# Kernel tuning notes

Hardware: AMD Instinct MI355X
Metric: run time of the kernel (lower is better)

## Reference

```python
import jax, jax.numpy as jnp
import numpy as np

N_NODES = 50000; N_EDGES = 800000
N_GRAPHS = 50; NODES_PER_GRAPH = 1000  # equal-size graphs: to_dense_batch == reshape
D_UNI = 1024; PE = 16; CH = 80; E_EMB = 16
D_STATE = 16; D_CONV = 4; DT_RANK = 5  # ceil(80/16)


def sinpe(pos, d):
    # interleaved sin/cos: even cols sin, odd cols cos
    den = jnp.power(10000.0, 2.0 * jnp.arange(d // 2, dtype=jnp.float32) / d)
    ang = pos[:, None] / den
    return jnp.stack([jnp.sin(ang), jnp.cos(ang)], -1).reshape(pos.shape[0], d)


def batchnorm(h, w, b, m, v):
    # eval-mode BatchNorm1d with running stats
    return (h - m) * jax.lax.rsqrt(v + 1e-5) * w + b


def gat_conv(x, src, dst, eattr, W, att_s, att_d, W_e, att_e, bias):
    # PyG GATConv (heads=1, add_self_loops=True, fill_value='mean', eval mode)
    N = x.shape[0]
    cnt = jax.ops.segment_sum(jnp.ones(src.shape[0], x.dtype), dst, N)
    loop_attr = jax.ops.segment_sum(eattr, dst, N) / jnp.maximum(cnt, 1.0)[:, None]
    idx = jnp.arange(N, dtype=src.dtype)
    src = jnp.concatenate([src, idx]); dst = jnp.concatenate([dst, idx])
    ea = jnp.concatenate([eattr, loop_attr], 0)
    h = x @ W                                   # [N, CH]
    a_s = h @ att_s; a_d = h @ att_d            # [N]
    a_e = (ea @ W_e) @ att_e                    # [E+N]
    alpha = jax.nn.leaky_relu(a_s[src] + a_d[dst] + a_e, negative_slope=0.2)
    amax = jax.ops.segment_max(alpha, dst, N)   # every node has a self loop
    ex = jnp.exp(alpha - amax[dst])
    denom = jax.ops.segment_sum(ex, dst, N)
    w = ex / denom[dst]
    out = jax.ops.segment_sum(w[:, None] * h[src], dst, N)
    return out + bias


def mamba(h, in_W, conv_w, conv_b, xp_W, dt_W, dt_b, A_log, D_p, out_W):
    # mamba_ssm Mamba(d_model=CH, d_state=16, d_conv=4, expand=1), all linears bias-free
    B, L, _ = h.shape
    xz = h @ in_W                               # [B, L, 2*CH]
    xc, z = jnp.split(xz, 2, -1)
    xpad = jnp.pad(xc, ((0, 0), (D_CONV - 1, 0), (0, 0)))
    xconv = conv_b
    for k in range(D_CONV):                     # depthwise causal conv, K=4
        xconv = xconv + xpad[:, k:k + L, :] * conv_w[:, k]
    u = jax.nn.silu(xconv)                      # [B, L, CH]
    proj = u @ xp_W                             # [B, L, DT_RANK + 2*D_STATE]
    dt, Bm, Cm = jnp.split(proj, [DT_RANK, DT_RANK + D_STATE], -1)
    dt = jax.nn.softplus(dt @ dt_W + dt_b)      # [B, L, CH]
    A = -jnp.exp(A_log)                         # [CH, D_STATE]
    dA = jnp.exp(dt[..., None] * A)             # [B, L, CH, D_STATE]
    dBu = dt[..., None] * Bm[:, :, None, :] * u[..., None]

    def step(hst, inp):
        dA_t, dBu_t, C_t = inp
        hst = dA_t * hst + dBu_t                # [B, CH, D_STATE]
        return hst, jnp.einsum('bds,bs->bd', hst, C_t)

    h0 = jnp.zeros((B, xc.shape[-1], D_STATE), h.dtype)
    _, ys = jax.lax.scan(step, h0, (jnp.moveaxis(dA, 1, 0), jnp.moveaxis(dBu, 1, 0), jnp.moveaxis(Cm, 1, 0)))
    y = jnp.moveaxis(ys, 0, 1) + u * D_p
    y = y * jax.nn.silu(z)
    return y @ out_W


def _forward(x, edge_index, ea_cat, ea_cont, W_uni, b_uni, edge_emb, W_edge, b_edge,
             gat_W, gat_as, gat_ad, gat_We, gat_ae, gat_b,
             bn1_w, bn1_b, bn1_m, bn1_v, bn2_w, bn2_b, bn2_m, bn2_v, bn3_w, bn3_b, bn3_m, bn3_v,
             m_in_W, m_conv_w, m_conv_b, m_xp_W, m_dt_W, m_dt_b, m_Alog, m_D, m_out_W,
             mlp_W1, mlp_b1, mlp_W2, mlp_b2, f_W1, f_b1, f_W2, f_b2, f_W3, f_b3):
    xf = x[:, 2:2 + D_UNI] @ W_uni + b_uni      # [N, 64]
    pe = jnp.concatenate([sinpe(x[:, 0], PE // 2), sinpe(x[:, 1], PE // 2)], -1)
    h = jnp.concatenate([xf, pe], 1)            # [N, 80]
    eattr = ea_cont @ W_edge + b_edge + edge_emb[ea_cat]
    src, dst = edge_index[0], edge_index[1]
    # GATMambaBlock (eval: dropouts identity)
    hg = gat_conv(h, src, dst, eattr, gat_W, gat_as, gat_ad, gat_We, gat_ae, gat_b)
    hg = batchnorm(hg, bn1_w, bn1_b, bn1_m, bn1_v)
    hd = h.reshape(N_GRAPHS, NODES_PER_GRAPH, CH)
    hm = mamba(hd, m_in_W, m_conv_w, m_conv_b, m_xp_W, m_dt_W, m_dt_b, m_Alog, m_D, m_out_W)
    hm = batchnorm(hm.reshape(N_NODES, CH), bn2_w, bn2_b, bn2_m, bn2_v)
    out = hg + hm
    out = out + (jax.nn.relu(out @ mlp_W1 + mlp_b1) @ mlp_W2 + mlp_b2)
    out = batchnorm(out, bn3_w, bn3_b, bn3_m, bn3_v)
    out = jax.nn.relu(out)
    pooled = out.reshape(N_GRAPHS, NODES_PER_GRAPH, CH).mean(1)  # global_mean_pool
    h1 = jax.nn.relu(pooled @ f_W1 + f_b1)
    h2 = jax.nn.relu(h1 @ f_W2 + f_b2)
    pred = h2 @ f_W3 + f_b3
    return pred, pooled


def setup_inputs() -> dict:
    ks = iter(jax.random.split(jax.random.key(0), 64))
    def nrm(shape, scale):
        return jax.random.normal(next(ks), shape, jnp.float32) * scale
    inp = {}
    inp['x'] = jnp.concatenate([jax.random.uniform(next(ks), (N_NODES, 2)) * 100.0,
                                nrm((N_NODES, D_UNI), 1.0)], 1)
    inp['edge_index'] = jax.random.randint(next(ks), (2, N_EDGES), 0, N_NODES, jnp.int32)
    inp['ea_cat'] = jax.random.randint(next(ks), (N_EDGES,), 0, 21, jnp.int32)
    inp['ea_cont'] = nrm((N_EDGES, 2), 1.0)
    inp['W_uni'] = nrm((D_UNI, 64), 0.03); inp['b_uni'] = jnp.zeros((64,))
    inp['edge_emb'] = nrm((21, E_EMB), 1.0)
    inp['W_edge'] = nrm((2, E_EMB), 0.5); inp['b_edge'] = jnp.zeros((E_EMB,))
    inp['gat_W'] = nrm((CH, CH), 0.1); inp['gat_as'] = nrm((CH,), 0.1); inp['gat_ad'] = nrm((CH,), 0.1)
    inp['gat_We'] = nrm((E_EMB, CH), 0.1); inp['gat_ae'] = nrm((CH,), 0.1); inp['gat_b'] = jnp.zeros((CH,))
    for i in (1, 2, 3):
        inp[f'bn{i}_w'] = jnp.ones((CH,)); inp[f'bn{i}_b'] = jnp.zeros((CH,))
        inp[f'bn{i}_m'] = nrm((CH,), 0.1)
        inp[f'bn{i}_v'] = jax.random.uniform(next(ks), (CH,), minval=0.5, maxval=1.5)
    inp['m_in_W'] = nrm((CH, 2 * CH), 0.1)
    inp['m_conv_w'] = nrm((CH, D_CONV), 0.3); inp['m_conv_b'] = jnp.zeros((CH,))
    inp['m_xp_W'] = nrm((CH, DT_RANK + 2 * D_STATE), 0.1)
    inp['m_dt_W'] = nrm((DT_RANK, CH), 0.3); inp['m_dt_b'] = nrm((CH,), 0.1)
    inp['m_Alog'] = jnp.log(jnp.tile(jnp.arange(1, D_STATE + 1, dtype=jnp.float32), (CH, 1)))
    inp['m_D'] = jnp.ones((CH,)); inp['m_out_W'] = nrm((CH, CH), 0.1)
    inp['mlp_W1'] = nrm((CH, 2 * CH), 0.1); inp['mlp_b1'] = jnp.zeros((2 * CH,))
    inp['mlp_W2'] = nrm((2 * CH, CH), 0.1); inp['mlp_b2'] = jnp.zeros((CH,))
    inp['f_W1'] = nrm((CH, CH // 2), 0.15); inp['f_b1'] = jnp.zeros((CH // 2,))
    inp['f_W2'] = nrm((CH // 2, CH // 4), 0.2); inp['f_b2'] = jnp.zeros((CH // 4,))
    inp['f_W3'] = nrm((CH // 4, 1), 0.3); inp['f_b3'] = jnp.zeros((1,))
    return inp


def reference(x, edge_index, ea_cat, ea_cont, W_uni, b_uni, edge_emb, W_edge, b_edge,
              gat_W, gat_as, gat_ad, gat_We, gat_ae, gat_b,
              bn1_w, bn1_b, bn1_m, bn1_v, bn2_w, bn2_b, bn2_m, bn2_v, bn3_w, bn3_b, bn3_m, bn3_v,
              m_in_W, m_conv_w, m_conv_b, m_xp_W, m_dt_W, m_dt_b, m_Alog, m_D, m_out_W,
              mlp_W1, mlp_b1, mlp_W2, mlp_b2, f_W1, f_b1, f_W2, f_b2, f_W3, f_b3):
    return _forward(x, edge_index, ea_cat, ea_cont, W_uni, b_uni, edge_emb, W_edge, b_edge,
                    gat_W, gat_as, gat_ad, gat_We, gat_ae, gat_b,
                    bn1_w, bn1_b, bn1_m, bn1_v, bn2_w, bn2_b, bn2_m, bn2_v, bn3_w, bn3_b, bn3_m, bn3_v,
                    m_in_W, m_conv_w, m_conv_b, m_xp_W, m_dt_W, m_dt_b, m_Alog, m_D, m_out_W,
                    mlp_W1, mlp_b1, mlp_W2, mlp_b2, f_W1, f_b1, f_W2, f_b2, f_W3, f_b3)
```

## Files before the change

### kernel.cpp

```cpp
#include <hip/hip_runtime.h>
#include <hip/hip_bf16.h>
#include <cstdint>

#define NNODES 50000
#define NEDGES 800000
#define NGRAPHS 50
#define NPG 1000
#define NB_SCAN 196
#define NCHUNK 10
#define CLEN 100

#define CO_WEAE 0
#define CO_WEC2 16
#define CO_BES  18
#define CO_EMBS 20
#define CO_WS   48
#define CO_WD   128
#define CO_BN1S 208
#define CO_BN1SH 288
#define CO_BN2S 368
#define CO_BN2SH 448
#define CO_BN3S 528
#define CO_BN3SH 608

__device__ __forceinline__ float lrelu(float x){ return x >= 0.f ? x : 0.2f*x; }
__device__ __forceinline__ float siluf(float x){ return x / (1.f + __expf(-x)); }

__device__ __forceinline__ int wave_incl_scan(int v) {
    int lane = threadIdx.x & 63;
    #pragma unroll
    for (int d = 1; d < 64; d <<= 1) {
        int o = __shfl_up(v, d, 64);
        if (lane >= d) v += o;
    }
    return v;
}

__global__ __launch_bounds__(256) void k_precompute(
        const float* __restrict__ gat_W, const float* __restrict__ gat_as, const float* __restrict__ gat_ad,
        const float* __restrict__ gat_We, const float* __restrict__ gat_ae,
        const float* __restrict__ W_edge, const float* __restrict__ b_edge, const float* __restrict__ edge_emb,
        const float* __restrict__ bn1_w, const float* __restrict__ bn1_b, const float* __restrict__ bn1_m, const float* __restrict__ bn1_v,
        const float* __restrict__ bn2_w, const float* __restrict__ bn2_b, const float* __restrict__ bn2_m, const float* __restrict__ bn2_v,
        const float* __restrict__ bn3_w, const float* __restrict__ bn3_b, const float* __restrict__ bn3_m, const float* __restrict__ bn3_v,
        float* __restrict__ consts)
{
    __shared__ float weae[16];
    int tid = threadIdx.x;
    if (tid < 16) {
        float s = 0.f;
        for (int c = 0; c < 80; ++c) s += gat_We[tid*80 + c] * gat_ae[c];
        weae[tid] = s;
        consts[CO_WEAE + tid] = s;
    }
    __syncthreads();
    if (tid < 2) {
        float s = 0.f;
        for (int k = 0; k < 16; ++k) s += W_edge[tid*16 + k] * weae[k];
        consts[CO_WEC2 + tid] = s;
    } else if (tid == 2) {
        float s = 0.f;
        for (int k = 0; k < 16; ++k) s += b_edge[k] * weae[k];
        consts[CO_BES] = s;
    }
    if (tid >= 32 && tid < 53) {
        int j = tid - 32;
        float s = 0.f;
        for (int k = 0; k < 16; ++k) s += edge_emb[j*16 + k] * weae[k];
        consts[CO_EMBS + j] = s;
    }
    if (tid >= 64 && tid < 144) {
        int r = tid - 64;
        float s1 = 0.f, s2 = 0.f;
        for (int c = 0; c < 80; ++c) {
            float w = gat_W[r*80 + c];
            s1 += w * gat_as[c];
            s2 += w * gat_ad[c];
        }
        consts[CO_WS + r] = s1;
        consts[CO_WD + r] = s2;
    }
    if (tid >= 160 && tid < 240) {
        int c = tid - 160;
        float sc1 = bn1_w[c] / sqrtf(bn1_v[c] + 1e-5f);
        consts[CO_BN1S + c] = sc1; consts[CO_BN1SH + c] = bn1_b[c] - bn1_m[c]*sc1;
        float sc2 = bn2_w[c] / sqrtf(bn2_v[c] + 1e-5f);
        consts[CO_BN2S + c] = sc2; consts[CO_BN2SH + c] = bn2_b[c] - bn2_m[c]*sc2;
        float sc3 = bn3_w[c] / sqrtf(bn3_v[c] + 1e-5f);
        consts[CO_BN3S + c] = sc3; consts[CO_BN3SH + c] = bn3_b[c] - bn3_m[c]*sc3;
    }
}

__global__ __launch_bounds__(256) void k_feat(const float* __restrict__ x,
        const float* __restrict__ W, const float* __restrict__ b,
        float* __restrict__ h)
{
    __shared__ float As[32][68];
    __shared__ float Bs[32][64];
    int tid = threadIdx.x;
    int node0 = blockIdx.x * 64;
    int tx = tid & 15, ty = tid >> 4;
    float acc[4][4] = {};
    int lr = tid >> 2;
    int lk = (tid & 3) * 8;
    int bk = tid >> 3;
    int bc = (tid & 7) * 8;
    for (int kk = 0; kk < 1024; kk += 32) {
        int n = node0 + lr;
        if (n < NNODES) {
            const float* xp = x + (size_t)n*1026 + 2 + kk + lk;
            #pragma unroll
            for (int j = 0; j < 8; ++j) As[lk+j][lr] = xp[j];
        } else {
            #pragma unroll
            for (int j = 0; j < 8; ++j) As[lk+j][lr] = 0.f;
        }
        const float* wp = W + (size_t)(kk+bk)*64 + bc;
        #pragma unroll
        for (int j = 0; j < 8; ++j) Bs[bk][bc+j] = wp[j];
        __syncthreads();
        #pragma unroll 8
        for (int i = 0; i < 32; ++i) {
            const float4 a  = *(const float4*)&As[i][ty*4];
            const float4 bb = *(const float4*)&Bs[i][tx*4];
            float av[4] = {a.x, a.y, a.z, a.w};
            float bv[4] = {bb.x, bb.y, bb.z, bb.w};
            #pragma unroll
            for (int r = 0; r < 4; ++r)
                #pragma unroll
                for (int j = 0; j < 4; ++j)
                    acc[r][j] = fmaf(av[r], bv[j], acc[r][j]);
        }
        __syncthreads();
    }
    #pragma unroll
    for (int r = 0; r < 4; ++r) {
        int n = node0 + ty*4 + r;
        if (n < NNODES) {
            #pragma unroll
            for (int j = 0; j < 4; ++j) {
                int c = tx*4 + j;
                h[(size_t)n*80 + c] = acc[r][j] + b[c];
            }
        }
    }
    for (int idx = tid; idx < 64*16; idx += 256) {
        int row = idx >> 4, col = idx & 15;
        int n = node0 + row;
        if (n < NNODES) {
            float pos = x[(size_t)n*1026 + (col < 8 ? 0 : 1)];
            int jj = (col & 7) >> 1;
            const float dens[4] = {1.f, 10.f, 100.f, 1000.f};
            float ang = pos / dens[jj];
            float v = (col & 1) ? cosf(ang) : sinf(ang);
            h[(size_t)n*80 + 64 + col] = v;
        }
    }
}

template<int K, int C, int RPT, int EPI>
__global__ __launch_bounds__(320) void k_gemm_rows(const float* __restrict__ in,
        const float* __restrict__ W, float* __restrict__ out, float* __restrict__ out2,
        const float* __restrict__ extra, const float* __restrict__ consts, int N)
{
    constexpr int GROUPS = 320 / C;
    constexpr int NPB = GROUPS * RPT;
    __shared__ float rows[NPB][K];
    int tid = threadIdx.x;
    int n0 = blockIdx.x * NPB;
    for (int idx = tid; idx < NPB*K; idx += 320) {
        int r = idx / K, k = idx - r*K;
        int n = n0 + r;
        rows[r][k] = (n < N) ? in[(size_t)n*K + k] : 0.f;
    }
    __syncthreads();
    int c = tid % C, grp = tid / C;
    float acc[RPT];
    #pragma unroll
    for (int r = 0; r < RPT; ++r) acc[r] = 0.f;
    #pragma unroll 4
    for (int k = 0; k < K; ++k) {
        float w = W[(size_t)k*C + c];
        #pragma unroll
        for (int r = 0; r < RPT; ++r) acc[r] = fmaf(rows[grp*RPT + r][k], w, acc[r]);
    }
    #pragma unroll
    for (int r = 0; r < RPT; ++r) {
        int n = n0 + grp*RPT + r;
        if (n >= N) continue;
        float v = acc[r];
        if (EPI == 0) {
            out[(size_t)n*C + c] = v;
        } else if (EPI == 1) {
            if (c < 80) out[(size_t)n*80 + c] = v;
            else        out2[(size_t)n*80 + (c-80)] = siluf(v);
        } else if (EPI == 2) {
            float bv = consts[CO_BN2S + c]*v + consts[CO_BN2SH + c] + extra[(size_t)n*80 + c];
            out[(size_t)n*80 + c] = bv;
        }
    }
}

__global__ __launch_bounds__(256) void k_edge_scalar(const float* __restrict__ ea_cont,
        const int* __restrict__ ea_cat, const int* __restrict__ dst,
        const float* __restrict__ consts, float* __restrict__ a_e,
        float* __restrict__ sum_ae, int* __restrict__ cnt)
{
    int e = blockIdx.x * 256 + threadIdx.x;
    if (e >= NEDGES) return;
    float2 ec = ((const float2*)ea_cont)[e];
    float v = ec.x*consts[CO_WEC2] + ec.y*consts[CO_WEC2+1] + consts[CO_BES]
            + consts[CO_EMBS + ea_cat[e]];
    a_e[e] = v;
    int d = dst[e];
    atomicAdd(sum_ae + d, v);
    atomicAdd(cnt + d, 1);
}

__global__ __launch_bounds__(256) void k_node_as(const float* __restrict__ h,
        const float* __restrict__ consts, const float* __restrict__ sum_ae,
        const int* __restrict__ cnt, float* __restrict__ a_s, float* __restrict__ a_d,
        float* __restrict__ alpha_self)
{
    __shared__ float wsv[80], wdv[80];
    int tid = threadIdx.x;
    if (tid < 80) { wsv[tid] = consts[CO_WS + tid]; wdv[tid] = consts[CO_WD + tid]; }
    __syncthreads();
    int n = blockIdx.x * 256 + tid;
    if (n >= NNODES) return;
    const float4* hr = (const float4*)(h + (size_t)n*80);
    float as = 0.f, ad = 0.f;
    #pragma unroll 5
    for (int i = 0; i < 20; ++i) {
        float4 f = hr[i];
        as += f.x*wsv[i*4] + f.y*wsv[i*4+1] + f.z*wsv[i*4+2] + f.w*wsv[i*4+3];
        ad += f.x*wdv[i*4] + f.y*wdv[i*4+1] + f.z*wdv[i*4+2] + f.w*wdv[i*4+3];
    }
    float aes = sum_ae[n] / fmaxf((float)cnt[n], 1.f);
    a_s[n] = as; a_d[n] = ad;
    alpha_self[n] = lrelu(as + ad + aes);
}

__global__ __launch_bounds__(256) void k_psum1(const int* __restrict__ cnt, int* __restrict__ bsum)
{
    __shared__ int ws4[4];
    int tid = threadIdx.x;
    int n = blockIdx.x*256 + tid;
    int v = (n < NNODES) ? cnt[n] : 0;
    int s = wave_incl_scan(v);
    if ((tid & 63) == 63) ws4[tid >> 6] = s;
    __syncthreads();
    if (tid == 0) {
        int t = 0;
        for (int w = 0; w < 4; ++w) t += ws4[w];
        bsum[blockIdx.x] = t;
    }
}

__global__ __launch_bounds__(256) void k_psum2(int* __restrict__ bsum)
{
    __shared__ int wsum[4], woff[4];
    int tid = threadIdx.x;
    int v = (tid < NB_SCAN) ? bsum[tid] : 0;
    int s = wave_incl_scan(v);
    if ((tid & 63) == 63) wsum[tid >> 6] = s;
    __syncthreads();
    if (tid == 0) { int r = 0; for (int w = 0; w < 4; ++w) { woff[w] = r; r += wsum[w]; } }
    __syncthreads();
    int excl = s - v + woff[tid >> 6];
    if (tid < NB_SCAN) bsum[tid] = excl;
}

__global__ __launch_bounds__(256) void k_psum3(const int* __restrict__ cnt,
        const int* __restrict__ bsum, int* __restrict__ rowptr, int* __restrict__ cursor)
{
    __shared__ int wsum[4], woff[4];
    int tid = threadIdx.x;
    int n = blockIdx.x*256 + tid;
    int v = (n < NNODES) ? cnt[n] : 0;
    int s = wave_incl_scan(v);
    if ((tid & 63) == 63) wsum[tid >> 6] = s;
    __syncthreads();
    if (tid == 0) { int r = 0; for (int w = 0; w < 4; ++w) { woff[w] = r; r += wsum[w]; } }
    __syncthreads();
    int excl = s - v + woff[tid >> 6] + bsum[blockIdx.x];
    if (n < NNODES) { rowptr[n] = excl; cursor[n] = excl; }
}

__global__ __launch_bounds__(256) void k_bucket(const int* __restrict__ src,
        const int* __restrict__ dst, const float* __restrict__ a_s,
        const float* __restrict__ a_d, const float* __restrict__ a_e,
        int* __restrict__ cursor, int2* __restrict__ ebuf)
{
    int e = blockIdx.x*256 + threadIdx.x;
    if (e >= NEDGES) return;
    int sN = src[e], d = dst[e];
    float al = lrelu(a_s[sN] + a_d[d] + a_e[e]);
    int pos = atomicAdd(cursor + d, 1);
    ebuf[pos] = make_int2(sN, __float_as_int(al));
}

__global__ __launch_bounds__(256) void k_gat_agg(const int* __restrict__ rowptr,
        const int* __restrict__ cnt, const int2* __restrict__ ebuf,
        const float* __restrict__ alpha_self, const float* __restrict__ hg,
        const float* __restrict__ gat_b, const float* __restrict__ consts,
        float* __restrict__ hgbn)
{
    int tid = threadIdx.x;
    int grp = tid >> 4, l = tid & 15;
    int n = blockIdx.x*16 + grp;
    if (n >= NNODES) return;
    int r0 = rowptr[n], c = cnt[n];
    float aself = alpha_self[n];
    float m = aself;
    for (int i = l; i < c; i += 16)
        m = fmaxf(m, __int_as_float(ebuf[r0 + i].y));
    m = fmaxf(m, __shfl_xor(m, 1, 16));
    m = fmaxf(m, __shfl_xor(m, 2, 16));
    m = fmaxf(m, __shfl_xor(m, 4, 16));
    m = fmaxf(m, __shfl_xor(m, 8, 16));
    float ex0 = __expf(aself - m);
    float denom = ex0;
    float acc[5];
    const float* hn = hg + (size_t)n*80;
    #pragma unroll
    for (int j = 0; j < 5; ++j) acc[j] = ex0 * hn[l + 16*j];
    for (int i = 0; i < c; ++i) {
        int2 p = ebuf[r0 + i];
        float ex = __expf(__int_as_float(p.y) - m);
        denom += ex;
        const float* hs = hg + (size_t)p.x*80;
        #pragma unroll
        for (int j = 0; j < 5; ++j) acc[j] = fmaf(ex, hs[l + 16*j], acc[j]);
    }
    float inv = 1.f/denom;
    #pragma unroll
    for (int j = 0; j < 5; ++j) {
        int ch = l + 16*j;
        float v = acc[j]*inv + gat_b[ch];
        hgbn[(size_t)n*80 + ch] = consts[CO_BN1S + ch]*v + consts[CO_BN1SH + ch];
    }
}

__global__ __launch_bounds__(256) void k_conv_proj(const float* __restrict__ xc,
        const float* __restrict__ conv_w, const float* __restrict__ conv_b,
        const float* __restrict__ xp_W, const float* __restrict__ dt_W,
        const float* __restrict__ dt_b, float* __restrict__ u_g,
        float* __restrict__ Bm, float* __restrict__ Cm, float* __restrict__ dt_g)
{
    __shared__ float us[40][80];
    __shared__ float dtr[40][5];
    int g = blockIdx.x / 25, chunk = blockIdx.x % 25;
    int t0 = chunk * 40;
    int tid = threadIdx.x;
    size_t gbase = (size_t)g * NPG;
    for (int idx = tid; idx < 40*80; idx += 256) {
        int t = idx / 80, d = idx - t*80;
        int tt = t0 + t;
        float acc = conv_b[d];
        #pragma unroll
        for (int k = 0; k < 4; ++k) {
            int ti = tt - 3 + k;
            float xv = (ti >= 0) ? xc[(gbase + ti)*80 + d] : 0.f;
            acc = fmaf(xv, conv_w[d*4 + k], acc);
        }
        float uv = siluf(acc);
        us[t][d] = uv;
        u_g[(gbase + tt)*80 + d] = uv;
    }
    __syncthreads();
    for (int idx = tid; idx < 40*37; idx += 256) {
        int t = idx / 37, j = idx - t*37;
        float acc = 0.f;
        #pragma unroll 4
        for (int k = 0; k < 80; ++k) acc = fmaf(us[t][k], xp_W[k*37 + j], acc);
        int tt = t0 + t;
        if (j < 5) dtr[t][j] = acc;
        else if (j < 21) Bm[(gbase + tt)*16 + (j-5)] = acc;
        else Cm[(gbase + tt)*16 + (j-21)] = acc;
    }
    __syncthreads();
    for (int idx = tid; idx < 40*80; idx += 256) {
        int t = idx / 80, d = idx - t*80;
        float acc = dt_b[d];
        #pragma unroll
        for (int r = 0; r < 5; ++r) acc = fmaf(dtr[t][r], dt_W[r*80 + d], acc);
        float sp = (acc > 20.f) ? acc : log1pf(__expf(acc));
        dt_g[(gbase + t0 + t)*80 + d] = sp;
    }
}

__global__ __launch_bounds__(256) void k_scan_a(const float* __restrict__ dt,
        const float* __restrict__ u, const float* __restrict__ Bm,
        const float* __restrict__ A_log, float* __restrict__ Pb, float* __restrict__ Qb)
{
    int b = blockIdx.x;
    int c = b % NCHUNK; int gd = b / NCHUNK;
    int g = gd / 5, dblk = gd % 5;
    int dl = threadIdx.x >> 4, s = threadIdx.x & 15;
    int d = dblk*16 + dl;
    float a = -__expf(A_log[d*16 + s]);
    size_t base80 = (size_t)g*NPG*80 + (size_t)c*CLEN*80 + d;
    size_t base16 = (size_t)g*NPG*16 + (size_t)c*CLEN*16 + s;
    float P = 1.f, Q = 0.f;
    for (int t = 0; t < CLEN; ++t) {
        float dtv = dt[base80 + (size_t)t*80];
        float uv  = u [base80 + (size_t)t*80];
        float Bv  = Bm[base16 + (size_t)t*16];
        float dA = __expf(dtv * a);
        Q = fmaf(dA, Q, dtv*uv*Bv);
        P *= dA;
    }
    size_t o = ((size_t)(g*NCHUNK + c)*80 + d)*16 + s;
    Pb[o] = P; Qb[o] = Q;
}

__global__ __launch_bounds__(256) void k_scan_c(const float* __restrict__ dt,
        const float* __restrict__ u, const float* __restrict__ Bm,
        const float* __restrict__ Cm, const float* __restrict__ A_log,
        const float* __restrict__ Dp, const float* __restrict__ sz,
        const float* __restrict__ Pb, const float* __restrict__ Qb,
        float* __restrict__ yraw)
{
    int b = blockIdx.x;
    int c = b % NCHUNK; int gd = b / NCHUNK;
    int g = gd / 5, dblk = gd % 5;
    int dl = threadIdx.x >> 4, s = threadIdx.x & 15;
    int d = dblk*16 + dl;
    float a = -__expf(A_log[d*16 + s]);
    float Dd = Dp[d];
    float hst = 0.f;
    for (int cc = 0; cc < c; ++cc) {
        size_t o = ((size_t)(g*NCHUNK + cc)*80 + d)*16 + s;
        hst = fmaf(Pb[o], hst, Qb[o]);
    }
    size_t base80 = (size_t)g*NPG*80 + (size_t)c*CLEN*80 + d;
    size_t base16 = (size_t)g*NPG*16 + (size_t)c*CLEN*16 + s;
    for (int t = 0; t < CLEN; ++t) {
        float dtv = dt[base80 + (size_t)t*80];
        float uv  = u [base80 + (size_t)t*80];
        float Bv  = Bm[base16 + (size_t)t*16];
        float Cv  = Cm[base16 + (size_t)t*16];
        float dA = __expf(dtv * a);
        hst = fmaf(dA, hst, dtv*uv*Bv);
        float cv = hst * Cv;
        cv += __shfl_xor(cv, 1, 16);
        cv += __shfl_xor(cv, 2, 16);
        cv += __shfl_xor(cv, 4, 16);
        cv += __shfl_xor(cv, 8, 16);
        if (s == 0) {
            size_t i = base80 + (size_t)t*80;
            yraw[i] = (cv + uv*Dd) * sz[i];
        }
    }
}

__global__ __launch_bounds__(640) void k_mlp(const float* __restrict__ s1,
        const float* __restrict__ W1, const float* __restrict__ b1,
        const float* __restrict__ W2, const float* __restrict__ b2,
        const float* __restrict__ consts, float* __restrict__ pooled)
{
    __shared__ float s1s[4][80];
    __shared__ float t1s[4][160];
    int tid = threadIdx.x;
    int n0 = blockIdx.x * 4;
    if (tid < 320) {
        int r = tid / 80, c = tid - r*80;
        s1s[r][c] = s1[(size_t)(n0 + r)*80 + c];
    }
    __syncthreads();
    {
        int r = tid / 160, j = tid - (tid/160)*160;
        float acc = b1[j];
        #pragma unroll 4
        for (int k = 0; k < 80; ++k) acc = fmaf(s1s[r][k], W1[k*160 + j], acc);
        t1s[r][j] = fmaxf(acc, 0.f);
    }
    __syncthreads();
    if (tid < 320) {
        int r = tid / 80, c = tid - (tid/80)*80;
        float acc = b2[c];
        #pragma unroll 4
        for (int k = 0; k < 160; ++k) acc = fmaf(t1s[r][k], W2[k*80 + c], acc);
        float v = s1s[r][c] + acc;
        v = consts[CO_BN3S + c]*v + consts[CO_BN3SH + c];
        v = fmaxf(v, 0.f);
        s1s[r][c] = v;
    }
    __syncthreads();
    if (tid < 80) {
        float sum = s1s[0][tid] + s1s[1][tid] + s1s[2][tid] + s1s[3][tid];
        atomicAdd(pooled + (n0 / NPG)*80 + tid, sum);
    }
}

__global__ __launch_bounds__(256) void k_pool_final(const float* __restrict__ pooled,
        const float* __restrict__ f_W1, const float* __restrict__ f_b1,
        const float* __restrict__ f_W2, const float* __restrict__ f_b2,
        const float* __restrict__ f_W3, const float* __restrict__ f_b3,
        float* __restrict__ d_out)
{
    __shared__ float pl[50*80];
    __shared__ float h1[50*40];
    __shared__ float h2[50*20];
    int tid = threadIdx.x;
    for (int idx = tid; idx < 50*80; idx += 256) {
        float v = pooled[idx] * (1.f/NPG);
        pl[idx] = v;
        d_out[50 + idx] = v;
    }
    __syncthreads();
    for (int idx = tid; idx < 50*40; idx += 256) {
        int g = idx / 40, j = idx - g*40;
        float acc = f_b1[j];
        for (int k = 0; k < 80; ++k) acc = fmaf(pl[g*80+k], f_W1[k*40+j], acc);
        h1[idx] = fmaxf(acc, 0.f);
    }
    __syncthreads();
    for (int idx = tid; idx < 50*20; idx += 256) {
        int g = idx / 20, j = idx - g*20;
        float acc = f_b2[j];
        for (int k = 0; k < 40; ++k) acc = fmaf(h1[g*40+k], f_W2[k*20+j], acc);
        h2[idx] = fmaxf(acc, 0.f);
    }
    __syncthreads();
    if (tid < 50) {
        float acc = f_b3[0];
        for (int k = 0; k < 20; ++k) acc = fmaf(h2[tid*20+k], f_W3[k], acc);
        d_out[tid] = acc;
    }
}

extern "C" void kernel_launch(void* const* d_in, const int* in_sizes, int n_in,
                              void* d_out, int out_size, void* d_ws, size_t ws_size,
                              hipStream_t stream)
{
    (void)in_sizes; (void)n_in; (void)out_size; (void)ws_size;
    const float* x        = (const float*)d_in[0];
    const int*   eidx     = (const int*)d_in[1];
    const int*   ea_cat   = (const int*)d_in[2];
    const float* ea_cont  = (const float*)d_in[3];
    const float* W_uni    = (const float*)d_in[4];
    const float* b_uni    = (const float*)d_in[5];
    const float* edge_emb = (const float*)d_in[6];
    const float* W_edge   = (const float*)d_in[7];
    const float* b_edge   = (const float*)d_in[8];
    const float* gat_W    = (const float*)d_in[9];
    const float* gat_as   = (const float*)d_in[10];
    const float* gat_ad   = (const float*)d_in[11];
    const float* gat_We   = (const float*)d_in[12];
    const float* gat_ae   = (const float*)d_in[13];
    const float* gat_b    = (const float*)d_in[14];
    const float* bn1_w = (const float*)d_in[15]; const float* bn1_b = (const float*)d_in[16];
    const float* bn1_m = (const float*)d_in[17]; const float* bn1_v = (const float*)d_in[18];
    const float* bn2_w = (const float*)d_in[19]; const float* bn2_b = (const float*)d_in[20];
    const float* bn2_m = (const float*)d_in[21]; const float* bn2_v = (const float*)d_in[22];
    const float* bn3_w = (const float*)d_in[23]; const float* bn3_b = (const float*)d_in[24];
    const float* bn3_m = (const float*)d_in[25]; const float* bn3_v = (const float*)d_in[26];
    const float* m_in_W   = (const float*)d_in[27];
    const float* m_conv_w = (const float*)d_in[28];
    const float* m_conv_b = (const float*)d_in[29];
    const float* m_xp_W   = (const float*)d_in[30];
    const float* m_dt_W   = (const float*)d_in[31];
    const float* m_dt_b   = (const float*)d_in[32];
    const float* m_Alog   = (const float*)d_in[33];
    const float* m_D      = (const float*)d_in[34];
    const float* m_out_W  = (const float*)d_in[35];
    const float* mlp_W1 = (const float*)d_in[36]; const float* mlp_b1 = (const float*)d_in[37];
    const float* mlp_W2 = (const float*)d_in[38]; const float* mlp_b2 = (const float*)d_in[39];
    const float* f_W1 = (const float*)d_in[40]; const float* f_b1 = (const float*)d_in[41];
    const float* f_W2 = (const float*)d_in[42]; const float* f_b2 = (const float*)d_in[43];
    const float* f_W3 = (const float*)d_in[44]; const float* f_b3 = (const float*)d_in[45];

    const int* src = eidx;
    const int* dst = eidx + NEDGES;

    float* wsf = (float*)d_ws;
    const size_t NN80 = (size_t)NNODES*80;
    size_t O_CONSTS = 0;
    size_t O_SUMAE  = 1024;
    size_t O_CNT    = O_SUMAE + NNODES;
    size_t O_POOLED = O_CNT + NNODES;
    size_t O_AE     = O_POOLED + 4000;
    size_t O_AS     = O_AE + NEDGES;
    size_t O_AD     = O_AS + NNODES;
    size_t O_ASELF  = O_AD + NNODES;
    size_t O_ROWPTR = O_ASELF + NNODES;
    size_t O_CURSOR = O_ROWPTR + NNODES;
    size_t O_BSUM   = O_CURSOR + NNODES;
    size_t O_EBUF   = O_BSUM + 256;
    size_t O_PB     = O_EBUF;
    size_t O_QB     = O_EBUF + 640000;
    size_t O_H      = O_EBUF + 2*(size_t)NEDGES;
    size_t O_HG     = O_H + NN80;
    size_t O_HGBN   = O_HG + NN80;
    size_t O_XC     = O_HGBN + NN80;
    size_t O_SZ     = O_XC + NN80;
    size_t O_U      = O_SZ + NN80;
    size_t O_DT     = O_U + NN80;
    size_t O_BM     = O_DT + NN80;
    size_t O_CM     = O_BM + (size_t)NNODES*16;

    hipMemsetAsync(wsf + O_SUMAE, 0, (2*(size_t)NNODES + 4000)*sizeof(float), stream);

    k_precompute<<<1, 256, 0, stream>>>(gat_W, gat_as, gat_ad, gat_We, gat_ae,
        W_edge, b_edge, edge_emb,
        bn1_w, bn1_b, bn1_m, bn1_v, bn2_w, bn2_b, bn2_m, bn2_v, bn3_w, bn3_b, bn3_m, bn3_v,
        wsf + O_CONSTS);

    k_feat<<<(NNODES + 63)/64, 256, 0, stream>>>(x, W_uni, b_uni, wsf + O_H);

    k_edge_scalar<<<(NEDGES + 255)/256, 256, 0, stream>>>(ea_cont, ea_cat, dst,
        wsf + O_CONSTS, wsf + O_AE, wsf + O_SUMAE, (int*)(wsf + O_CNT));

    k_gemm_rows<80, 80, 8, 0><<<(NNODES + 31)/32, 320, 0, stream>>>(
        wsf + O_H, gat_W, wsf + O_HG, nullptr, nullptr, wsf + O_CONSTS, NNODES);

    k_node_as<<<(NNODES + 255)/256, 256, 0, stream>>>(wsf + O_H, wsf + O_CONSTS,
        wsf + O_SUMAE, (const int*)(wsf + O_CNT), wsf + O_AS, wsf + O_AD, wsf + O_ASELF);

    k_psum1<<<NB_SCAN, 256, 0, stream>>>((const int*)(wsf + O_CNT), (int*)(wsf + O_BSUM));
    k_psum2<<<1, 256, 0, stream>>>((int*)(wsf + O_BSUM));
    k_psum3<<<NB_SCAN, 256, 0, stream>>>((const int*)(wsf + O_CNT),
        (const int*)(wsf + O_BSUM), (int*)(wsf + O_ROWPTR), (int*)(wsf + O_CURSOR));

    k_bucket<<<(NEDGES + 255)/256, 256, 0, stream>>>(src, dst, wsf + O_AS,
        wsf + O_AD, wsf + O_AE, (int*)(wsf + O_CURSOR), (int2*)(wsf + O_EBUF));

    k_gat_agg<<<NNODES/16, 256, 0, stream>>>((const int*)(wsf + O_ROWPTR),
        (const int*)(wsf + O_CNT), (const int2*)(wsf + O_EBUF), wsf + O_ASELF,
        wsf + O_HG, gat_b, wsf + O_CONSTS, wsf + O_HGBN);

    k_gemm_rows<80, 160, 8, 1><<<(NNODES + 15)/16, 320, 0, stream>>>(
        wsf + O_H, m_in_W, wsf + O_XC, wsf + O_SZ, nullptr, wsf + O_CONSTS, NNODES);

    k_conv_proj<<<NGRAPHS*25, 256, 0, stream>>>(wsf + O_XC, m_conv_w, m_conv_b,
        m_xp_W, m_dt_W, m_dt_b, wsf + O_U, wsf + O_BM, wsf + O_CM, wsf + O_DT);

    k_scan_a<<<NGRAPHS*5*NCHUNK, 256, 0, stream>>>(wsf + O_DT, wsf + O_U,
        wsf + O_BM, m_Alog, wsf + O_PB, wsf + O_QB);

    k_scan_c<<<NGRAPHS*5*NCHUNK, 256, 0, stream>>>(wsf + O_DT, wsf + O_U,
        wsf + O_BM, wsf + O_CM, m_Alog, m_D, wsf + O_SZ,
        wsf + O_PB, wsf + O_QB, wsf + O_HG );

    k_gemm_rows<80, 80, 8, 2><<<(NNODES + 31)/32, 320, 0, stream>>>(
        wsf + O_HG , m_out_W, wsf + O_H , nullptr,
        wsf + O_HGBN, wsf + O_CONSTS, NNODES);

    k_mlp<<<NNODES/4, 640, 0, stream>>>(wsf + O_H , mlp_W1, mlp_b1,
        mlp_W2, mlp_b2, wsf + O_CONSTS, wsf + O_POOLED);

    k_pool_final<<<1, 256, 0, stream>>>(wsf + O_POOLED, f_W1, f_b1, f_W2, f_b2,
        f_W3, f_b3, (float*)d_out);
}
```

Before: 1.233 ms.

## Split fused MLP into register-tiled GEMM kernels and a per-graph pooling kernel

The fused per-4-row MLP kernel is replaced by two instances of the register-tiled row GEMM kernel, each computing 8 rows per thread, with new epilogues for bias+ReLU and for bias+residual+BN+ReLU. The aim is to get far more reuse of each weight load than the old kernel, which reloaded W1 and W2 for every group of four nodes. Mean pooling now runs in a dedicated per-graph reduction kernel instead of global atomics, so the pooled buffer no longer needs zeroing. The cost is that the 160-wide hidden activation and the MLP output make a round trip through global memory, reusing the buffers previously held by HGBN/XC and SZ.

```diff
diff --git a/kernel.cpp b/kernel.cpp
--- a/kernel.cpp
+++ b/kernel.cpp
@@ -161,7 +161,8 @@
 template<int K, int C, int RPT, int EPI>
 __global__ __launch_bounds__(320) void k_gemm_rows(const float* __restrict__ in,
         const float* __restrict__ W, float* __restrict__ out, float* __restrict__ out2,
-        const float* __restrict__ extra, const float* __restrict__ consts, int N)
+        const float* __restrict__ extra, const float* __restrict__ bias,
+        const float* __restrict__ consts, int N)
 {
     constexpr int GROUPS = 320 / C;
     constexpr int NPB = GROUPS * RPT;
@@ -197,6 +198,12 @@
         } else if (EPI == 2) {
             float bv = consts[CO_BN2S + c]*v + consts[CO_BN2SH + c] + extra[(size_t)n*80 + c];
             out[(size_t)n*80 + c] = bv;
+        } else if (EPI == 3) {
+            out[(size_t)n*C + c] = fmaxf(v + bias[c], 0.f);
+        } else if (EPI == 4) {
+            float bv = v + bias[c] + extra[(size_t)n*80 + c];
+            bv = consts[CO_BN3S + c]*bv + consts[CO_BN3SH + c];
+            out[(size_t)n*80 + c] = fmaxf(bv, 0.f);
         }
     }
 }
@@ -455,43 +462,21 @@
     }
 }
 
-__global__ __launch_bounds__(640) void k_mlp(const float* __restrict__ s1,
-        const float* __restrict__ W1, const float* __restrict__ b1,
-        const float* __restrict__ W2, const float* __restrict__ b2,
-        const float* __restrict__ consts, float* __restrict__ pooled)
-{
-    __shared__ float s1s[4][80];
-    __shared__ float t1s[4][160];
-    int tid = threadIdx.x;
-    int n0 = blockIdx.x * 4;
-    if (tid < 320) {
-        int r = tid / 80, c = tid - r*80;
-        s1s[r][c] = s1[(size_t)(n0 + r)*80 + c];
-    }
-    __syncthreads();
-    {
-        int r = tid / 160, j = tid - (tid/160)*160;
-        float acc = b1[j];
-        #pragma unroll 4
-        for (int k = 0; k < 80; ++k) acc = fmaf(s1s[r][k], W1[k*160 + j], acc);
-        t1s[r][j] = fmaxf(acc, 0.f);
-    }
-    __syncthreads();
-    if (tid < 320) {
-        int r = tid / 80, c = tid - (tid/80)*80;
-        float acc = b2[c];
-        #pragma unroll 4
-        for (int k = 0; k < 160; ++k) acc = fmaf(t1s[r][k], W2[k*80 + c], acc);
-        float v = s1s[r][c] + acc;
-        v = consts[CO_BN3S + c]*v + consts[CO_BN3SH + c];
-        v = fmaxf(v, 0.f);
-        s1s[r][c] = v;
-    }
-    __syncthreads();
-    if (tid < 80) {
-        float sum = s1s[0][tid] + s1s[1][tid] + s1s[2][tid] + s1s[3][tid];
-        atomicAdd(pooled + (n0 / NPG)*80 + tid, sum);
-    }
+__global__ __launch_bounds__(320) void k_pool(const float* __restrict__ s2,
+        float* __restrict__ pooled)
+{
+    __shared__ float part[4][80];
+    int g = blockIdx.x;
+    int tid = threadIdx.x;
+    int c = tid % 80, rg = tid / 80;
+    float sum = 0.f;
+    const float* base = s2 + (size_t)g*NPG*80;
+    for (int r = rg; r < NPG; r += 4)
+        sum += base[(size_t)r*80 + c];
+    part[rg][c] = sum;
+    __syncthreads();
+    if (tid < 80)
+        pooled[g*80 + tid] = part[0][tid] + part[1][tid] + part[2][tid] + part[3][tid];
 }
 
 __global__ __launch_bounds__(256) void k_pool_final(const float* __restrict__ pooled,
@@ -600,8 +585,10 @@
     size_t O_DT     = O_U + NN80;
     size_t O_BM     = O_DT + NN80;
     size_t O_CM     = O_BM + (size_t)NNODES*16;
-
-    hipMemsetAsync(wsf + O_SUMAE, 0, (2*(size_t)NNODES + 4000)*sizeof(float), stream);
+    size_t O_T1     = O_HGBN;
+    size_t O_S2     = O_SZ;
+
+    hipMemsetAsync(wsf + O_SUMAE, 0, 2*(size_t)NNODES*sizeof(float), stream);
 
     k_precompute<<<1, 256, 0, stream>>>(gat_W, gat_as, gat_ad, gat_We, gat_ae,
         W_edge, b_edge, edge_emb,
@@ -614,7 +601,7 @@
         wsf + O_CONSTS, wsf + O_AE, wsf + O_SUMAE, (int*)(wsf + O_CNT));
 
     k_gemm_rows<80, 80, 8, 0><<<(NNODES + 31)/32, 320, 0, stream>>>(
-        wsf + O_H, gat_W, wsf + O_HG, nullptr, nullptr, wsf + O_CONSTS, NNODES);
+        wsf + O_H, gat_W, wsf + O_HG, nullptr, nullptr, nullptr, wsf + O_CONSTS, NNODES);
 
     k_node_as<<<(NNODES + 255)/256, 256, 0, stream>>>(wsf + O_H, wsf + O_CONSTS,
         wsf + O_SUMAE, (const int*)(wsf + O_CNT), wsf + O_AS, wsf + O_AD, wsf + O_ASELF);
@@ -632,7 +619,7 @@
         wsf + O_HG, gat_b, wsf + O_CONSTS, wsf + O_HGBN);
 
     k_gemm_rows<80, 160, 8, 1><<<(NNODES + 15)/16, 320, 0, stream>>>(
-        wsf + O_H, m_in_W, wsf + O_XC, wsf + O_SZ, nullptr, wsf + O_CONSTS, NNODES);
+        wsf + O_H, m_in_W, wsf + O_XC, wsf + O_SZ, nullptr, nullptr, wsf + O_CONSTS, NNODES);
 
     k_conv_proj<<<NGRAPHS*25, 256, 0, stream>>>(wsf + O_XC, m_conv_w, m_conv_b,
         m_xp_W, m_dt_W, m_dt_b, wsf + O_U, wsf + O_BM, wsf + O_CM, wsf + O_DT);
@@ -646,10 +633,17 @@
 
     k_gemm_rows<80, 80, 8, 2><<<(NNODES + 31)/32, 320, 0, stream>>>(
         wsf + O_HG , m_out_W, wsf + O_H , nullptr,
-        wsf + O_HGBN, wsf + O_CONSTS, NNODES);
-
-    k_mlp<<<NNODES/4, 640, 0, stream>>>(wsf + O_H , mlp_W1, mlp_b1,
-        mlp_W2, mlp_b2, wsf + O_CONSTS, wsf + O_POOLED);
+        wsf + O_HGBN, nullptr, wsf + O_CONSTS, NNODES);
+
+    k_gemm_rows<80, 160, 8, 3><<<(NNODES + 15)/16, 320, 0, stream>>>(
+        wsf + O_H , mlp_W1, wsf + O_T1, nullptr, nullptr, mlp_b1,
+        wsf + O_CONSTS, NNODES);
+
+    k_gemm_rows<160, 80, 8, 4><<<(NNODES + 31)/32, 320, 0, stream>>>(
+        wsf + O_T1, mlp_W2, wsf + O_S2, nullptr, wsf + O_H , mlp_b2,
+        wsf + O_CONSTS, NNODES);
+
+    k_pool<<<NGRAPHS, 320, 0, stream>>>(wsf + O_S2, wsf + O_POOLED);
 
     k_pool_final<<<1, 256, 0, stream>>>(wsf + O_POOLED, f_W1, f_b1, f_W2, f_b2,
         f_W3, f_b3, (float*)d_out);
```

Measured after the change: 1.113 ms. -9.7%, faster.
